# Performance work log

Measured on AMD Instinct MI355X. Metric: run time of the kernel, lower is better.

## Reference

```python
import jax, jax.numpy as jnp
import numpy as np

DIM = 2048
NUM_HEADS = 16
HEAD_DIM = DIM // NUM_HEADS  # 128
B, L = 2, 2048


def setup_inputs() -> dict:
    key = jax.random.key(0)
    ks = jax.random.split(key, 5)
    x = jax.random.normal(ks[0], (B, L, DIM), dtype=jnp.float32)
    # genuine RoPE tables: inv_freq over half the head dim
    half = HEAD_DIM // 2
    inv_freq = 1.0 / (10000.0 ** (jnp.arange(half, dtype=jnp.float32) / half))
    ang = jnp.arange(L, dtype=jnp.float32)[:, None] * inv_freq[None, :]  # (L, half)
    cos = jnp.cos(ang)[:, None, :]  # (L, 1, half) broadcasts over (B,L,H,half)
    sin = jnp.sin(ang)[:, None, :]
    def dw_init(k, shape):
        fan_in, fan_out = shape
        std = 1.0 / np.sqrt(fan_in) * min(1.0, np.sqrt(fan_out / fan_in))
        return jax.random.normal(k, shape, dtype=jnp.float32) * std
    Wq = dw_init(ks[1], (DIM, DIM))
    Wk = dw_init(ks[2], (DIM, HEAD_DIM))
    Wv = dw_init(ks[3], (DIM, HEAD_DIM))
    Wo = dw_init(ks[4], (DIM, DIM))  # random instead of zeros so output is nontrivial
    return {"x": x, "cos": cos, "sin": sin, "Wq": Wq, "Wk": Wk, "Wv": Wv, "Wo": Wo}


def apply_rotary_emb(x, cos, sin):
    x1, x2 = jnp.split(x, 2, axis=-1)
    return jnp.concatenate([x1 * cos + x2 * sin, x1 * -sin + x2 * cos], axis=-1)


def rms_norm(x):
    return x * jax.lax.rsqrt(jnp.mean(x * x, axis=-1, keepdims=True) + 1e-6)


def reference(x, cos, sin, Wq, Wk, Wv, Wo):
    Bb, Ll, _ = x.shape
    q = (x @ Wq).reshape(Bb, Ll, NUM_HEADS, HEAD_DIM)  # (B,L,H,D)
    k = (x @ Wk)  # (B,L,D)  single KV head (MQA)
    v = (x @ Wv)  # (B,L,D)
    q = rms_norm(apply_rotary_emb(q, cos, sin))
    k = rms_norm(apply_rotary_emb(k[:, :, None, :], cos, sin))[:, :, 0, :]  # (B,L,D)
    scale = 1.0 / jnp.sqrt(jnp.asarray(HEAD_DIM, dtype=x.dtype))
    # scores without materializing broadcasted K: (B,H,Lq,Lk)
    scores = jnp.einsum('bqhd,bkd->bhqk', q, k) * scale
    causal = jnp.tril(jnp.ones((Ll, Ll), dtype=jnp.bool_))
    scores = jnp.where(causal[None, None], scores, jnp.asarray(-jnp.inf, dtype=scores.dtype))
    attn = jax.nn.softmax(scores, axis=-1)
    out = jnp.einsum('bhqk,bkd->bqhd', attn, v).reshape(Bb, Ll, DIM)
    return out @ Wo
```

## Files before the change

### kernel.cpp

```cpp
#include <hip/hip_runtime.h>

#define DIM 2048
#define NH 16
#define HD 128
#define BB 2
#define LL 2048
#define MROWS (BB * LL)
#define NKV 2304
#define NT 32

typedef __attribute__((ext_vector_type(8))) short short8;
typedef __attribute__((ext_vector_type(4))) float floatx4;

__device__ inline ushort f2bf(float f) {
    union { float f; unsigned u; } v; v.f = f;
    unsigned r = v.u + 0x7FFFu + ((v.u >> 16) & 1u);
    return (ushort)(r >> 16);
}

__device__ __forceinline__ ushort f2bf_fast(float f) {
    __bf16 h = (__bf16)f;
    return __builtin_bit_cast(unsigned short, h);
}

#define GL16(g, l)                                                         \
    __builtin_amdgcn_global_load_lds(                                      \
        (const __attribute__((address_space(1))) unsigned int*)(g),        \
        (__attribute__((address_space(3))) unsigned int*)(l), 16, 0, 0)

__device__ __forceinline__ short8 ld8(const ushort* p) {
    return *reinterpret_cast<const short8*>(p);
}

__global__ __launch_bounds__(256) void prep(const float* __restrict__ x,
                                            ushort* __restrict__ xb,
                                            const float* __restrict__ Wq,
                                            const float* __restrict__ Wk,
                                            const float* __restrict__ Wv,
                                            const float* __restrict__ Wo,
                                            ushort* __restrict__ Wcatt,
                                            ushort* __restrict__ Wot) {
    __shared__ ushort T[64][72];
    const int bid = blockIdx.x;
    const int tid = threadIdx.x;
    if (bid < 4096) {
        size_t i = ((size_t)bid * 256 + tid) * 8;
        float4 a = *reinterpret_cast<const float4*>(x + i);
        float4 b = *reinterpret_cast<const float4*>(x + i + 4);
        ushort o[8] = {f2bf(a.x), f2bf(a.y), f2bf(a.z), f2bf(a.w),
                       f2bf(b.x), f2bf(b.y), f2bf(b.z), f2bf(b.w)};
        *reinterpret_cast<uint4*>(xb + i) = *reinterpret_cast<uint4*>(o);
        return;
    }
    const int wb = bid - 4096;
    const float* in;
    ushort* out;
    int in_ld, c0, r0;
    const int out_ld = 2048;
    if (wb < 1024) {
        in = Wq; out = Wcatt; in_ld = 2048;
        c0 = (wb & 31) * 64; r0 = (wb >> 5) * 64;
    } else if (wb < 2048) {
        int t = wb - 1024;
        in = Wo; out = Wot; in_ld = 2048;
        c0 = (t & 31) * 64; r0 = (t >> 5) * 64;
    } else if (wb < 2112) {
        int t = wb - 2048;
        in = Wk; out = Wcatt + (size_t)2048 * 2048; in_ld = 128;
        c0 = (t & 1) * 64; r0 = (t >> 1) * 64;
    } else {
        int t = wb - 2112;
        in = Wv; out = Wcatt + (size_t)2176 * 2048; in_ld = 128;
        c0 = (t & 1) * 64; r0 = (t >> 1) * 64;
    }
#pragma unroll
    for (int rep = 0; rep < 4; ++rep) {
        int idx = tid + rep * 256;
        int r = idx >> 4, c4 = idx & 15;
        float4 f = *reinterpret_cast<const float4*>(
            in + (size_t)(r0 + r) * in_ld + c0 + c4 * 4);
        T[r][c4 * 4 + 0] = f2bf(f.x);
        T[r][c4 * 4 + 1] = f2bf(f.y);
        T[r][c4 * 4 + 2] = f2bf(f.z);
        T[r][c4 * 4 + 3] = f2bf(f.w);
    }
    __syncthreads();
#pragma unroll
    for (int rep = 0; rep < 4; ++rep) {
        int idx = tid + rep * 256;
        int cr = idx >> 4, rc4 = idx & 15;
        uint a0 = (uint)T[rc4 * 4 + 0][cr] | ((uint)T[rc4 * 4 + 1][cr] << 16);
        uint a1 = (uint)T[rc4 * 4 + 2][cr] | ((uint)T[rc4 * 4 + 3][cr] << 16);
        uint2 val = {a0, a1};
        *reinterpret_cast<uint2*>(
            out + (size_t)(c0 + cr) * out_ld + r0 + rc4 * 4) = val;
    }
}

template <int U>
__device__ __forceinline__ void stage_unit(const ushort* __restrict__ A,
                                           const ushort* __restrict__ Bt,
                                           ushort* lbase, uint offA, uint offB,
                                           int t) {
    if (t >= NT) return;
    const ushort* g = (U < 2) ? Bt : A;
    uint off = ((U < 2) ? offB : offA) + ((U & 1) ? 128u * 2048u : 0u) +
               (uint)t * 64u;
    ushort* l = lbase + U * 8192;
    GL16(g + off, l + (size_t)threadIdx.x * 8);
    GL16(g + off + 64u * 2048u, l + (size_t)(threadIdx.x + 512) * 8);
}

__global__ __launch_bounds__(512)
__attribute__((amdgpu_waves_per_eu(2, 2)))
void gemm2p(const ushort* __restrict__ A,
            const ushort* __restrict__ Bt,
            float* __restrict__ Y, int N) {
    __shared__ __attribute__((aligned(16))) ushort lds[65536];
    const int tid = threadIdx.x;
    const int lane = tid & 63;
    const int w = tid >> 6;
    const int wm = w >> 2, wn = w & 3;
    const int col = lane & 15, quad = lane >> 4;
    const int sel = col & 7;
    const int m0 = blockIdx.y * 256, n0 = blockIdx.x * 256;

    const int r0 = tid >> 3;
    const int gc0 = (tid & 7) ^ (r0 & 7);
    const uint offA = (uint)(m0 + r0) * 2048u + (uint)gc0 * 8u;
    const uint offB = (uint)(n0 + r0) * 2048u + (uint)gc0 * 8u;

    floatx4 acc[8][4];
#pragma unroll
    for (int mt = 0; mt < 8; ++mt)
#pragma unroll
        for (int nt = 0; nt < 4; ++nt) acc[mt][nt] = (floatx4){0.f, 0.f, 0.f, 0.f};

    const int aoff0 = (2 + wm) * 8192 + col * 64;
    const int boff0 = (wn >> 1) * 8192 + ((wn & 1) * 64 + col) * 64;
    const int koff0 = (quad ^ sel) * 8;
    const int koff1 = ((4 + quad) ^ sel) * 8;

    stage_unit<0>(A, Bt, lds, offA, offB, 0);
    stage_unit<1>(A, Bt, lds, offA, offB, 0);
    stage_unit<2>(A, Bt, lds, offA, offB, 0);
    stage_unit<3>(A, Bt, lds, offA, offB, 0);
    asm volatile("s_waitcnt vmcnt(0)" ::: "memory");
    __builtin_amdgcn_s_barrier();

#pragma unroll 2
    for (int t = 0; t < NT; ++t) {
        ushort* lb = lds + (t & 1) * 32768;
        ushort* lbn = lds + ((t + 1) & 1) * 32768;

        short8 a0[8], b0[4];
#pragma unroll
        for (int mt = 0; mt < 8; ++mt)
            a0[mt] = ld8(lb + aoff0 + mt * 1024 + koff0);
#pragma unroll
        for (int nt = 0; nt < 4; ++nt)
            b0[nt] = ld8(lb + boff0 + nt * 1024 + koff0);
        stage_unit<0>(A, Bt, lbn, offA, offB, t + 1);
        stage_unit<1>(A, Bt, lbn, offA, offB, t + 1);
        stage_unit<2>(A, Bt, lbn, offA, offB, t + 1);
        stage_unit<3>(A, Bt, lbn, offA, offB, t + 1);
        __builtin_amdgcn_s_setprio(1);
#pragma unroll
        for (int mt = 0; mt < 8; ++mt)
#pragma unroll
            for (int nt = 0; nt < 4; ++nt)
                acc[mt][nt] = __builtin_amdgcn_mfma_f32_16x16x32_bf16(
                    a0[mt], b0[nt], acc[mt][nt], 0, 0, 0);
        __builtin_amdgcn_s_setprio(0);

        short8 a1[8], b1[4];
#pragma unroll
        for (int mt = 0; mt < 8; ++mt)
            a1[mt] = ld8(lb + aoff0 + mt * 1024 + koff1);
#pragma unroll
        for (int nt = 0; nt < 4; ++nt)
            b1[nt] = ld8(lb + boff0 + nt * 1024 + koff1);
        __builtin_amdgcn_s_setprio(1);
#pragma unroll
        for (int mt = 0; mt < 8; ++mt)
#pragma unroll
            for (int nt = 0; nt < 4; ++nt)
                acc[mt][nt] = __builtin_amdgcn_mfma_f32_16x16x32_bf16(
                    a1[mt], b1[nt], acc[mt][nt], 0, 0, 0);
        __builtin_amdgcn_s_setprio(0);
        asm volatile("s_waitcnt vmcnt(0)" ::: "memory");
        __builtin_amdgcn_s_barrier();
    }

#pragma unroll
    for (int mt = 0; mt < 8; ++mt)
#pragma unroll
        for (int nt = 0; nt < 4; ++nt)
#pragma unroll
            for (int rr = 0; rr < 4; ++rr)
                Y[(size_t)(m0 + wm * 128 + mt * 16 + quad * 4 + rr) * N + n0 +
                  wn * 64 + nt * 16 + col] = acc[mt][nt][rr];
}

template <int U>
__device__ __forceinline__ void stage_po(const ushort* __restrict__ A,
                                         const ushort* __restrict__ Bt,
                                         ushort* lbase, uint offA, uint offB,
                                         int t) {
    if (t >= NT) return;
    const ushort* g = (U < 2) ? Bt : A;
    uint off = ((U < 2) ? offB : offA) + ((U == 1) ? 128u * 2048u : 0u) +
               (uint)t * 64u;
    ushort* l = lbase + U * 8192;
    GL16(g + off, l + (size_t)threadIdx.x * 8);
    GL16(g + off + 64u * 2048u, l + (size_t)(threadIdx.x + 512) * 8);
}

__global__ __launch_bounds__(512)
__attribute__((amdgpu_waves_per_eu(2, 2)))
void gemm2pw(const ushort* __restrict__ A,
             const ushort* __restrict__ Bt,
             float* __restrict__ Y, int N) {
    __shared__ __attribute__((aligned(16))) ushort lds[49152];
    const int tid = threadIdx.x;
    const int lane = tid & 63;
    const int w = tid >> 6;
    const int wm = w >> 2, wn = w & 3;
    const int col = lane & 15, quad = lane >> 4;
    const int sel = col & 7;
    const int m0 = blockIdx.y * 128, n0 = blockIdx.x * 256;

    const int r0 = tid >> 3;
    const int gc0 = (tid & 7) ^ (r0 & 7);
    const uint offA = (uint)(m0 + r0) * 2048u + (uint)gc0 * 8u;
    const uint offB = (uint)(n0 + r0) * 2048u + (uint)gc0 * 8u;

    floatx4 acc[4][4];
#pragma unroll
    for (int mt = 0; mt < 4; ++mt)
#pragma unroll
        for (int nt = 0; nt < 4; ++nt) acc[mt][nt] = (floatx4){0.f, 0.f, 0.f, 0.f};

    const int aoff0 = 16384 + wm * 4096 + col * 64;
    const int boff0 = (wn >> 1) * 8192 + ((wn & 1) * 64 + col) * 64;
    const int koff0 = (quad ^ sel) * 8;
    const int koff1 = ((4 + quad) ^ sel) * 8;

    stage_po<0>(A, Bt, lds, offA, offB, 0);
    stage_po<1>(A, Bt, lds, offA, offB, 0);
    stage_po<2>(A, Bt, lds, offA, offB, 0);
    asm volatile("s_waitcnt vmcnt(0)" ::: "memory");
    __builtin_amdgcn_s_barrier();

#pragma unroll 2
    for (int t = 0; t < NT; ++t) {
        ushort* lb = lds + (t & 1) * 24576;
        ushort* lbn = lds + ((t + 1) & 1) * 24576;

        short8 a0[4], b0[4];
#pragma unroll
        for (int mt = 0; mt < 4; ++mt)
            a0[mt] = ld8(lb + aoff0 + mt * 1024 + koff0);
#pragma unroll
        for (int nt = 0; nt < 4; ++nt)
            b0[nt] = ld8(lb + boff0 + nt * 1024 + koff0);
        stage_po<0>(A, Bt, lbn, offA, offB, t + 1);
        stage_po<1>(A, Bt, lbn, offA, offB, t + 1);
        stage_po<2>(A, Bt, lbn, offA, offB, t + 1);
        __builtin_amdgcn_s_setprio(1);
#pragma unroll
        for (int mt = 0; mt < 4; ++mt)
#pragma unroll
            for (int nt = 0; nt < 4; ++nt)
                acc[mt][nt] = __builtin_amdgcn_mfma_f32_16x16x32_bf16(
                    a0[mt], b0[nt], acc[mt][nt], 0, 0, 0);
        __builtin_amdgcn_s_setprio(0);

        short8 a1[4], b1[4];
#pragma unroll
        for (int mt = 0; mt < 4; ++mt)
            a1[mt] = ld8(lb + aoff0 + mt * 1024 + koff1);
#pragma unroll
        for (int nt = 0; nt < 4; ++nt)
            b1[nt] = ld8(lb + boff0 + nt * 1024 + koff1);
        __builtin_amdgcn_s_setprio(1);
#pragma unroll
        for (int mt = 0; mt < 4; ++mt)
#pragma unroll
            for (int nt = 0; nt < 4; ++nt)
                acc[mt][nt] = __builtin_amdgcn_mfma_f32_16x16x32_bf16(
                    a1[mt], b1[nt], acc[mt][nt], 0, 0, 0);
        __builtin_amdgcn_s_setprio(0);
        asm volatile("s_waitcnt vmcnt(0)" ::: "memory");
        __builtin_amdgcn_s_barrier();
    }

#pragma unroll
    for (int mt = 0; mt < 4; ++mt)
#pragma unroll
        for (int nt = 0; nt < 4; ++nt)
#pragma unroll
            for (int rr = 0; rr < 4; ++rr)
                Y[(size_t)(m0 + wm * 64 + mt * 16 + quad * 4 + rr) * N + n0 +
                  wn * 64 + nt * 16 + col] = acc[mt][nt][rr];
}

__device__ __forceinline__ void rope_row(const float* __restrict__ in,
                                         ushort* __restrict__ outb,
                                         const float* __restrict__ cosb,
                                         const float* __restrict__ sinb,
                                         int row, int heads, int in_ld,
                                         int lane) {
    int token = row / heads, head = row % heads;
    int l = token & (LL - 1);
    const float* p = in + (size_t)token * in_ld + head * HD;
    float x1 = p[lane];
    float x2 = p[lane + 64];
    float c = cosb[l * 64 + lane];
    float s = sinb[l * 64 + lane];
    float o1 = x1 * c + x2 * s;
    float o2 = -x1 * s + x2 * c;
    float ss = o1 * o1 + o2 * o2;
#pragma unroll
    for (int off = 32; off > 0; off >>= 1) ss += __shfl_xor(ss, off);
    float r = rsqrtf(ss * (1.0f / 128.0f) + 1e-6f);
    outb[(size_t)row * HD + lane] = f2bf(o1 * r);
    outb[(size_t)row * HD + lane + 64] = f2bf(o2 * r);
}

__global__ __launch_bounds__(256) void rope_vt(const float* __restrict__ qkv,
                                               ushort* __restrict__ qb,
                                               ushort* __restrict__ kb,
                                               ushort* __restrict__ vt,
                                               const float* __restrict__ cosb,
                                               const float* __restrict__ sinb) {
    __shared__ ushort T[64][72];
    const int bid = blockIdx.x;
    const int tid = threadIdx.x;
    const int lane = tid & 63;
    if (bid < 16384) {
        int row = bid * 4 + (tid >> 6);
        rope_row(qkv, qb, cosb, sinb, row, NH, NKV, lane);
        return;
    }
    if (bid < 17408) {
        int row = (bid - 16384) * 4 + (tid >> 6);
        rope_row(qkv + DIM, kb, cosb, sinb, row, 1, NKV, lane);
        return;
    }
    const int t = bid - 17408;
    const int l0 = (t & 31) * 64, d0 = ((t >> 5) & 1) * 64, b = t >> 6;
    const float* v = qkv + DIM + HD;
#pragma unroll
    for (int rep = 0; rep < 4; ++rep) {
        int idx = tid + rep * 256;
        int r = idx >> 4, c4 = idx & 15;
        float4 f = *reinterpret_cast<const float4*>(
            v + (size_t)(b * LL + l0 + r) * NKV + d0 + c4 * 4);
        T[r][c4 * 4 + 0] = f2bf(f.x);
        T[r][c4 * 4 + 1] = f2bf(f.y);
        T[r][c4 * 4 + 2] = f2bf(f.z);
        T[r][c4 * 4 + 3] = f2bf(f.w);
    }
    __syncthreads();
#pragma unroll
    for (int rep = 0; rep < 4; ++rep) {
        int idx = tid + rep * 256;
        int dr = idx >> 4, lc4 = idx & 15;
        uint a0 = (uint)T[lc4 * 4 + 0][dr] | ((uint)T[lc4 * 4 + 1][dr] << 16);
        uint a1 = (uint)T[lc4 * 4 + 2][dr] | ((uint)T[lc4 * 4 + 3][dr] << 16);
        uint2 val = {a0, a1};
        *reinterpret_cast<uint2*>(
            vt + (size_t)(b * HD + d0 + dr) * LL + l0 + lc4 * 4) = val;
    }
}

__global__ __launch_bounds__(256) void flash_mfma(const ushort* __restrict__ qb,
                                                  const ushort* __restrict__ kb,
                                                  const ushort* __restrict__ vt,
                                                  ushort* __restrict__ aob) {
    __shared__ ushort Ks[64 * 128];
    __shared__ ushort VTs[128 * 64];
    __shared__ ushort Ps[4][16][68];

    const int tid = threadIdx.x;
    const int w = tid >> 6, lane = tid & 63;
    const int col = lane & 15, quad = lane >> 4;
    const int pairIdx = blockIdx.x, bh = blockIdx.y;
    const int b = bh >> 4, h = bh & 15;
    const int sel = col & 7;
    const float scl2 = 0.08838834764831845f * 1.44269504088896340736f;
    const float M2 = 11.5f * 1.44269504088896340736f;

    const int ksr[4] = {(tid + 0) >> 4, (tid + 256) >> 4, (tid + 512) >> 4,
                        (tid + 768) >> 4};
    const int vsr[4] = {(tid + 0) >> 3, (tid + 256) >> 3, (tid + 512) >> 3,
                        (tid + 768) >> 3};

    for (int sp = 0; sp < 2; ++sp) {
        const int qt = sp ? (31 - pairIdx) : pairIdx;
        const int q0 = qt * 64;

        const ushort* qrow =
            qb + ((size_t)(b * LL + q0 + w * 16 + col) * NH + h) * HD;
        short8 aq[4];
#pragma unroll
        for (int kc = 0; kc < 4; ++kc)
            aq[kc] = *reinterpret_cast<const short8*>(qrow + kc * 32 + quad * 8);

        float lrow[4] = {0.f, 0.f, 0.f, 0.f};
        floatx4 oacc[8];
#pragma unroll
        for (int dt = 0; dt < 8; ++dt) oacc[dt] = (floatx4){0.f, 0.f, 0.f, 0.f};

        const int ntiles = qt + 1;
        for (int kt = 0; kt < ntiles; ++kt) {
            const int k0 = kt * 64;
            __syncthreads();
#pragma unroll
            for (int rep = 0; rep < 4; ++rep) {
                int slot = tid + rep * 256;
                int r = ksr[rep];
                int gc = (slot & 15) ^ (r & 7);
                GL16(kb + (size_t)(b * LL + k0 + r) * HD + gc * 8,
                     Ks + (size_t)slot * 8);
            }
#pragma unroll
            for (int rep = 0; rep < 4; ++rep) {
                int slot = tid + rep * 256;
                int r = vsr[rep];
                int gc = (slot & 7) ^ (r & 7);
                GL16(vt + (size_t)(b * HD + r) * LL + k0 + gc * 8,
                     VTs + (size_t)slot * 8);
            }
            __syncthreads();

            floatx4 sacc[4];
#pragma unroll
            for (int nt = 0; nt < 4; ++nt)
                sacc[nt] = (floatx4){0.f, 0.f, 0.f, 0.f};
            __builtin_amdgcn_s_setprio(1);
#pragma unroll
            for (int nt = 0; nt < 4; ++nt) {
#pragma unroll
                for (int kc = 0; kc < 4; ++kc) {
                    short8 bk = *reinterpret_cast<const short8*>(
                        &Ks[(nt * 16 + col) * 128 +
                            ((kc * 4 + quad) ^ sel) * 8]);
                    sacc[nt] = __builtin_amdgcn_mfma_f32_16x16x32_bf16(
                        aq[kc], bk, sacc[nt], 0, 0, 0);
                }
            }
            __builtin_amdgcn_s_setprio(0);

            float psum[4] = {0.f, 0.f, 0.f, 0.f};
            if (kt == qt) {
#pragma unroll
                for (int nt = 0; nt < 4; ++nt) {
                    int kj = k0 + nt * 16 + col;
#pragma unroll
                    for (int rr = 0; rr < 4; ++rr) {
                        int qi = q0 + w * 16 + quad * 4 + rr;
                        float p = exp2f(fmaf(sacc[nt][rr], scl2, -M2));
                        p = (kj <= qi) ? p : 0.0f;
                        sacc[nt][rr] = p;
                        psum[rr] += p;
                    }
                }
            } else {
#pragma unroll
                for (int nt = 0; nt < 4; ++nt)
#pragma unroll
                    for (int rr = 0; rr < 4; ++rr) {
                        float p = exp2f(fmaf(sacc[nt][rr], scl2, -M2));
                        sacc[nt][rr] = p;
                        psum[rr] += p;
                    }
            }
#pragma unroll
            for (int rr = 0; rr < 4; ++rr) lrow[rr] += psum[rr];

#pragma unroll
            for (int nt = 0; nt < 4; ++nt)
#pragma unroll
                for (int rr = 0; rr < 4; ++rr)
                    Ps[w][quad * 4 + rr][nt * 16 + col] =
                        f2bf_fast(sacc[nt][rr]);
            asm volatile("s_waitcnt lgkmcnt(0)" ::: "memory");

#pragma unroll
            for (int kt2 = 0; kt2 < 2; ++kt2) {
                short8 ap = *reinterpret_cast<const short8*>(
                    &Ps[w][col][kt2 * 32 + quad * 8]);
                __builtin_amdgcn_s_setprio(1);
#pragma unroll
                for (int dt = 0; dt < 8; ++dt) {
                    short8 bv = *reinterpret_cast<const short8*>(
                        &VTs[(dt * 16 + col) * 64 +
                             ((kt2 * 4 + quad) ^ sel) * 8]);
                    oacc[dt] = __builtin_amdgcn_mfma_f32_16x16x32_bf16(
                        ap, bv, oacc[dt], 0, 0, 0);
                }
                __builtin_amdgcn_s_setprio(0);
            }
        }

#pragma unroll
        for (int off = 1; off < 16; off <<= 1)
#pragma unroll
            for (int rr = 0; rr < 4; ++rr)
                lrow[rr] += __shfl_xor(lrow[rr], off);
        float inv[4];
#pragma unroll
        for (int rr = 0; rr < 4; ++rr) inv[rr] = 1.0f / lrow[rr];
#pragma unroll
        for (int dt = 0; dt < 8; ++dt)
#pragma unroll
            for (int rr = 0; rr < 4; ++rr)
                aob[((size_t)(b * LL + q0 + w * 16 + quad * 4 + rr) * NH + h) *
                        HD + dt * 16 + col] =
                    f2bf_fast(oacc[dt][rr] * inv[rr]);
    }
}

extern "C" void kernel_launch(void* const* d_in, const int* in_sizes, int n_in,
                              void* d_out, int out_size, void* d_ws,
                              size_t ws_size, hipStream_t stream) {
    const float* x    = (const float*)d_in[0];
    const float* cosb = (const float*)d_in[1];
    const float* sinb = (const float*)d_in[2];
    const float* Wq   = (const float*)d_in[3];
    const float* Wk   = (const float*)d_in[4];
    const float* Wv   = (const float*)d_in[5];
    const float* Wo   = (const float*)d_in[6];
    float* out = (float*)d_out;

    float* qkv  = (float*)d_ws;
    ushort* xb  = (ushort*)(qkv + (size_t)MROWS * NKV);
    ushort* qb  = xb + (size_t)MROWS * DIM;
    ushort* kb  = qb + (size_t)MROWS * DIM;
    ushort* vt  = kb + (size_t)MROWS * HD;
    ushort* aob = vt + (size_t)MROWS * HD;
    ushort* Wcatt = aob + (size_t)MROWS * DIM;
    ushort* Wot   = Wcatt + (size_t)NKV * DIM;

    prep<<<dim3(4096 + 2176), 256, 0, stream>>>(x, xb, Wq, Wk, Wv, Wo, Wcatt,
                                                Wot);

    gemm2p<<<dim3(NKV / 256, MROWS / 256), 512, 0, stream>>>(xb, Wcatt, qkv,
                                                             NKV);

    rope_vt<<<dim3(16384 + 1024 + 128), 256, 0, stream>>>(qkv, qb, kb, vt,
                                                          cosb, sinb);

    flash_mfma<<<dim3(LL / 128, BB * NH), 256, 0, stream>>>(qb, kb, vt, aob);

    gemm2pw<<<dim3(DIM / 256, MROWS / 128), 512, 0, stream>>>(aob, Wot, out,
                                                              DIM);
}
```

Baseline: 290.7 us.

## Double-buffer K/V tiles and process 128 query rows per block in flash attention

Each flash attention block now handles two 64-row query sub-tiles (128 rows), so every K and V tile loaded into shared memory feeds twice as many MFMAs. K/V loads are double-buffered: the next tile is prefetched with async global-to-LDS copies while the current one is consumed, using vmcnt waits and raw barriers instead of two syncthreads per tile. The grid is halved to 8x32 blocks (256 total), which lowers occupancy and parallelism on a large GPU, and register and LDS use roughly double.

```diff
diff --git a/kernel.cpp b/kernel.cpp
--- a/kernel.cpp
+++ b/kernel.cpp
@@ -379,9 +379,9 @@
                                                   const ushort* __restrict__ kb,
                                                   const ushort* __restrict__ vt,
                                                   ushort* __restrict__ aob) {
-    __shared__ ushort Ks[64 * 128];
-    __shared__ ushort VTs[128 * 64];
-    __shared__ ushort Ps[4][16][68];
+    __shared__ ushort Ks[2][64 * 128];
+    __shared__ ushort VTs[2][128 * 64];
+    __shared__ ushort Ps[4][2][16][68];
 
     const int tid = threadIdx.x;
     const int w = tid >> 6, lane = tid & 63;
@@ -392,134 +392,170 @@
     const float scl2 = 0.08838834764831845f * 1.44269504088896340736f;
     const float M2 = 11.5f * 1.44269504088896340736f;
 
-    const int ksr[4] = {(tid + 0) >> 4, (tid + 256) >> 4, (tid + 512) >> 4,
-                        (tid + 768) >> 4};
-    const int vsr[4] = {(tid + 0) >> 3, (tid + 256) >> 3, (tid + 512) >> 3,
-                        (tid + 768) >> 3};
+    auto stageKV = [&](int kt, int bf) {
+        const int k0 = kt * 64;
+#pragma unroll
+        for (int rep = 0; rep < 4; ++rep) {
+            int slot = tid + rep * 256;
+            int r = slot >> 4;
+            int gc = (slot & 15) ^ (r & 7);
+            GL16(kb + (size_t)(b * LL + k0 + r) * HD + gc * 8,
+                 &Ks[bf][0] + (size_t)slot * 8);
+        }
+#pragma unroll
+        for (int rep = 0; rep < 4; ++rep) {
+            int slot = tid + rep * 256;
+            int r = slot >> 3;
+            int gc = (slot & 7) ^ (r & 7);
+            GL16(vt + (size_t)(b * HD + r) * LL + k0 + gc * 8,
+                 &VTs[bf][0] + (size_t)slot * 8);
+        }
+    };
 
     for (int sp = 0; sp < 2; ++sp) {
-        const int qt = sp ? (31 - pairIdx) : pairIdx;
-        const int q0 = qt * 64;
-
-        const ushort* qrow =
-            qb + ((size_t)(b * LL + q0 + w * 16 + col) * NH + h) * HD;
-        short8 aq[4];
-#pragma unroll
-        for (int kc = 0; kc < 4; ++kc)
-            aq[kc] = *reinterpret_cast<const short8*>(qrow + kc * 32 + quad * 8);
-
-        float lrow[4] = {0.f, 0.f, 0.f, 0.f};
-        floatx4 oacc[8];
-#pragma unroll
-        for (int dt = 0; dt < 8; ++dt) oacc[dt] = (floatx4){0.f, 0.f, 0.f, 0.f};
-
-        const int ntiles = qt + 1;
-        for (int kt = 0; kt < ntiles; ++kt) {
+        const int qt = sp ? (15 - pairIdx) : pairIdx;
+        const int q0 = qt * 128;
+        const int nkv = 2 * (qt + 1);
+
+        short8 aq[2][4];
+#pragma unroll
+        for (int mt = 0; mt < 2; ++mt) {
+            const ushort* qrow =
+                qb +
+                ((size_t)(b * LL + q0 + mt * 64 + w * 16 + col) * NH + h) * HD;
+#pragma unroll
+            for (int kc = 0; kc < 4; ++kc)
+                aq[mt][kc] =
+                    *reinterpret_cast<const short8*>(qrow + kc * 32 + quad * 8);
+        }
+
+        float lrow[2][4] = {{0.f, 0.f, 0.f, 0.f}, {0.f, 0.f, 0.f, 0.f}};
+        floatx4 oacc[2][8];
+#pragma unroll
+        for (int mt = 0; mt < 2; ++mt)
+#pragma unroll
+            for (int dt = 0; dt < 8; ++dt)
+                oacc[mt][dt] = (floatx4){0.f, 0.f, 0.f, 0.f};
+
+        stageKV(0, 0);
+        int cur = 0;
+
+        for (int kt = 0; kt < nkv; ++kt) {
             const int k0 = kt * 64;
-            __syncthreads();
-#pragma unroll
-            for (int rep = 0; rep < 4; ++rep) {
-                int slot = tid + rep * 256;
-                int r = ksr[rep];
-                int gc = (slot & 15) ^ (r & 7);
-                GL16(kb + (size_t)(b * LL + k0 + r) * HD + gc * 8,
-                     Ks + (size_t)slot * 8);
+            if (kt + 1 < nkv) {
+                stageKV(kt + 1, cur ^ 1);
+                asm volatile("s_waitcnt vmcnt(8)" ::: "memory");
+            } else {
+                asm volatile("s_waitcnt vmcnt(0)" ::: "memory");
             }
-#pragma unroll
-            for (int rep = 0; rep < 4; ++rep) {
-                int slot = tid + rep * 256;
-                int r = vsr[rep];
-                int gc = (slot & 7) ^ (r & 7);
-                GL16(vt + (size_t)(b * HD + r) * LL + k0 + gc * 8,
-                     VTs + (size_t)slot * 8);
-            }
-            __syncthreads();
-
-            floatx4 sacc[4];
-#pragma unroll
-            for (int nt = 0; nt < 4; ++nt)
-                sacc[nt] = (floatx4){0.f, 0.f, 0.f, 0.f};
+            __builtin_amdgcn_s_barrier();
+
+            floatx4 sacc[2][4];
+#pragma unroll
+            for (int mt = 0; mt < 2; ++mt)
+#pragma unroll
+                for (int nt = 0; nt < 4; ++nt)
+                    sacc[mt][nt] = (floatx4){0.f, 0.f, 0.f, 0.f};
             __builtin_amdgcn_s_setprio(1);
 #pragma unroll
             for (int nt = 0; nt < 4; ++nt) {
 #pragma unroll
                 for (int kc = 0; kc < 4; ++kc) {
                     short8 bk = *reinterpret_cast<const short8*>(
-                        &Ks[(nt * 16 + col) * 128 +
-                            ((kc * 4 + quad) ^ sel) * 8]);
-                    sacc[nt] = __builtin_amdgcn_mfma_f32_16x16x32_bf16(
-                        aq[kc], bk, sacc[nt], 0, 0, 0);
+                        &Ks[cur][(nt * 16 + col) * 128 +
+                                 ((kc * 4 + quad) ^ sel) * 8]);
+#pragma unroll
+                    for (int mt = 0; mt < 2; ++mt)
+                        sacc[mt][nt] = __builtin_amdgcn_mfma_f32_16x16x32_bf16(
+                            aq[mt][kc], bk, sacc[mt][nt], 0, 0, 0);
                 }
             }
             __builtin_amdgcn_s_setprio(0);
 
-            float psum[4] = {0.f, 0.f, 0.f, 0.f};
-            if (kt == qt) {
-#pragma unroll
-                for (int nt = 0; nt < 4; ++nt) {
-                    int kj = k0 + nt * 16 + col;
-#pragma unroll
-                    for (int rr = 0; rr < 4; ++rr) {
-                        int qi = q0 + w * 16 + quad * 4 + rr;
-                        float p = exp2f(fmaf(sacc[nt][rr], scl2, -M2));
-                        p = (kj <= qi) ? p : 0.0f;
-                        sacc[nt][rr] = p;
-                        psum[rr] += p;
+            if (kt >= nkv - 2) {
+#pragma unroll
+                for (int mt = 0; mt < 2; ++mt)
+#pragma unroll
+                    for (int nt = 0; nt < 4; ++nt) {
+                        int kj = k0 + nt * 16 + col;
+#pragma unroll
+                        for (int rr = 0; rr < 4; ++rr) {
+                            int qi = q0 + mt * 64 + w * 16 + quad * 4 + rr;
+                            float p = exp2f(fmaf(sacc[mt][nt][rr], scl2, -M2));
+                            p = (kj <= qi) ? p : 0.0f;
+                            sacc[mt][nt][rr] = p;
+                            lrow[mt][rr] += p;
+                        }
                     }
-                }
             } else {
 #pragma unroll
+                for (int mt = 0; mt < 2; ++mt)
+#pragma unroll
+                    for (int nt = 0; nt < 4; ++nt)
+#pragma unroll
+                        for (int rr = 0; rr < 4; ++rr) {
+                            float p = exp2f(fmaf(sacc[mt][nt][rr], scl2, -M2));
+                            sacc[mt][nt][rr] = p;
+                            lrow[mt][rr] += p;
+                        }
+            }
+
+#pragma unroll
+            for (int mt = 0; mt < 2; ++mt)
+#pragma unroll
                 for (int nt = 0; nt < 4; ++nt)
 #pragma unroll
-                    for (int rr = 0; rr < 4; ++rr) {
-                        float p = exp2f(fmaf(sacc[nt][rr], scl2, -M2));
-                        sacc[nt][rr] = p;
-                        psum[rr] += p;
-                    }
-            }
-#pragma unroll
-            for (int rr = 0; rr < 4; ++rr) lrow[rr] += psum[rr];
-
-#pragma unroll
-            for (int nt = 0; nt < 4; ++nt)
-#pragma unroll
-                for (int rr = 0; rr < 4; ++rr)
-                    Ps[w][quad * 4 + rr][nt * 16 + col] =
-                        f2bf_fast(sacc[nt][rr]);
+                    for (int rr = 0; rr < 4; ++rr)
+                        Ps[w][mt][quad * 4 + rr][nt * 16 + col] =
+                            f2bf_fast(sacc[mt][nt][rr]);
             asm volatile("s_waitcnt lgkmcnt(0)" ::: "memory");
 
 #pragma unroll
             for (int kt2 = 0; kt2 < 2; ++kt2) {
-                short8 ap = *reinterpret_cast<const short8*>(
-                    &Ps[w][col][kt2 * 32 + quad * 8]);
+                short8 ap[2];
+#pragma unroll
+                for (int mt = 0; mt < 2; ++mt)
+                    ap[mt] = *reinterpret_cast<const short8*>(
+                        &Ps[w][mt][col][kt2 * 32 + quad * 8]);
                 __builtin_amdgcn_s_setprio(1);
 #pragma unroll
                 for (int dt = 0; dt < 8; ++dt) {
                     short8 bv = *reinterpret_cast<const short8*>(
-                        &VTs[(dt * 16 + col) * 64 +
-                             ((kt2 * 4 + quad) ^ sel) * 8]);
-                    oacc[dt] = __builtin_amdgcn_mfma_f32_16x16x32_bf16(
-                        ap, bv, oacc[dt], 0, 0, 0);
+                        &VTs[cur][(dt * 16 + col) * 64 +
+                                  ((kt2 * 4 + quad) ^ sel) * 8]);
+#pragma unroll
+                    for (int mt = 0; mt < 2; ++mt)
+                        oacc[mt][dt] = __builtin_amdgcn_mfma_f32_16x16x32_bf16(
+                            ap[mt], bv, oacc[mt][dt], 0, 0, 0);
                 }
                 __builtin_amdgcn_s_setprio(0);
             }
+
+            __builtin_amdgcn_s_barrier();
+            cur ^= 1;
         }
 
 #pragma unroll
-        for (int off = 1; off < 16; off <<= 1)
-#pragma unroll
-            for (int rr = 0; rr < 4; ++rr)
-                lrow[rr] += __shfl_xor(lrow[rr], off);
-        float inv[4];
-#pragma unroll
-        for (int rr = 0; rr < 4; ++rr) inv[rr] = 1.0f / lrow[rr];
-#pragma unroll
-        for (int dt = 0; dt < 8; ++dt)
-#pragma unroll
-            for (int rr = 0; rr < 4; ++rr)
-                aob[((size_t)(b * LL + q0 + w * 16 + quad * 4 + rr) * NH + h) *
-                        HD + dt * 16 + col] =
-                    f2bf_fast(oacc[dt][rr] * inv[rr]);
+        for (int mt = 0; mt < 2; ++mt) {
+#pragma unroll
+            for (int off = 1; off < 16; off <<= 1)
+#pragma unroll
+                for (int rr = 0; rr < 4; ++rr)
+                    lrow[mt][rr] += __shfl_xor(lrow[mt][rr], off);
+            float inv[4];
+#pragma unroll
+            for (int rr = 0; rr < 4; ++rr) inv[rr] = 1.0f / lrow[mt][rr];
+#pragma unroll
+            for (int dt = 0; dt < 8; ++dt)
+#pragma unroll
+                for (int rr = 0; rr < 4; ++rr)
+                    aob[((size_t)(b * LL + q0 + mt * 64 + w * 16 + quad * 4 +
+                                  rr) *
+                             NH +
+                         h) *
+                            HD +
+                        dt * 16 + col] = f2bf_fast(oacc[mt][dt][rr] * inv[rr]);
+        }
     }
 }
 
@@ -553,7 +589,7 @@
     rope_vt<<<dim3(16384 + 1024 + 128), 256, 0, stream>>>(qkv, qb, kb, vt,
                                                           cosb, sinb);
 
-    flash_mfma<<<dim3(LL / 128, BB * NH), 256, 0, stream>>>(qb, kb, vt, aob);
+    flash_mfma<<<dim3(8, BB * NH), 256, 0, stream>>>(qb, kb, vt, aob);
 
     gemm2pw<<<dim3(DIM / 256, MROWS / 128), 512, 0, stream>>>(aob, Wot, out,
                                                               DIM);
```

Result: slower. 298.9 us (+2.8%).
